# Optimization experiments

Hardware: AMD Instinct MI355X
Metric: run time of the kernel (lower is better)

Reference implementation:

```python
import jax, jax.numpy as jnp
import numpy as np
import math

N_NODES = 1048576   # total rows of x
N_SEG = 8192        # number of hyperedges (segments)
D_IN = 128
D_H = 64            # hidden_dim == embed_dim of the MHA


def setup_inputs() -> dict:
    key = jax.random.key(0)
    ks = jax.random.split(key, 12)
    x = jax.random.normal(ks[0], (N_NODES, D_IN), dtype=jnp.float32)
    # offset: sorted, with fixed endpoints 0 and N_NODES (torch.split semantics)
    cuts = jnp.sort(jax.random.randint(ks[1], (N_SEG - 1,), 0, N_NODES, dtype=jnp.int32))
    offset = jnp.concatenate([jnp.zeros((1,), jnp.int32), cuts,
                              jnp.full((1,), N_NODES, jnp.int32)])
    s1 = 1.0 / math.sqrt(D_IN)
    s2 = 1.0 / math.sqrt(D_H)
    W1 = jax.random.normal(ks[2], (D_H, D_IN), jnp.float32) * s1
    b1 = jax.random.normal(ks[3], (D_H,), jnp.float32) * s1
    W2 = jax.random.normal(ks[4], (D_H, D_H), jnp.float32) * s2
    b2 = jax.random.normal(ks[5], (D_H,), jnp.float32) * s2
    in_proj_w = jax.random.normal(ks[6], (3 * D_H, D_H), jnp.float32) * s2
    in_proj_b = jax.random.normal(ks[7], (3 * D_H,), jnp.float32) * s2
    out_w = jax.random.normal(ks[8], (D_H, D_H), jnp.float32) * s2
    out_b = jax.random.normal(ks[9], (D_H,), jnp.float32) * s2
    return {"x": x, "offset": offset, "W1": W1, "b1": b1, "W2": W2, "b2": b2,
            "in_proj_w": in_proj_w, "in_proj_b": in_proj_b,
            "out_w": out_w, "out_b": out_b}


def reference(x, offset, W1, b1, W2, b2, in_proj_w, in_proj_b, out_w, out_b):
    n = x.shape[0]
    n_seg = offset.shape[0] - 1
    # phi MLP: Linear->ReLU->Linear->ReLU
    h = jax.nn.relu(x @ W1.T + b1)
    h = jax.nn.relu(h @ W2.T + b2)                      # [N, 64]
    # ragged segment-sum pooling (torch.split + per-slice sum, fused)
    seg_ids = jnp.searchsorted(offset, jnp.arange(n, dtype=offset.dtype),
                               side='right') - 1
    tokens = jax.ops.segment_sum(h, seg_ids, num_segments=n_seg)  # [S, 64]
    # MultiheadAttention with batch_first=False: input is [L=1, batch=S, E=64],
    # so each token attends over a length-1 sequence.
    Wq, Wk, Wv = jnp.split(in_proj_w, 3, axis=0)
    bq, bk, bv = jnp.split(in_proj_b, 3, axis=0)
    t = tokens[:, None, :]                               # [S, 1, E]
    q = t @ Wq.T + bq
    k = t @ Wk.T + bk
    v = t @ Wv.T + bv
    scale = 1.0 / math.sqrt(t.shape[-1])
    scores = jnp.einsum('sqe,ske->sqk', q, k) * scale    # [S, 1, 1]
    attn = jax.nn.softmax(scores, axis=-1)               # trivially ones
    ctx = jnp.einsum('sqk,ske->sqe', attn, v)[:, 0]      # [S, 64]
    return ctx @ out_w.T + out_b
```

## Files before the change

kernel.cpp:

```cpp
#include <hip/hip_runtime.h>
#include <math.h>

#define NNODES 1048576
#define NSEG   8192
#define DIN    128
#define DH     64

typedef __bf16 bf16x8 __attribute__((ext_vector_type(8)));
typedef float  f32x4  __attribute__((ext_vector_type(4)));

__global__ void seg_fill_kernel(const int* __restrict__ offset, int* __restrict__ seg_id) {
    int s = blockIdx.x;
    int start = offset[s], end = offset[s + 1];
    for (int i = start + (int)threadIdx.x; i < end; i += (int)blockDim.x) seg_id[i] = s;
}

__global__ void fold_kernel(const float* __restrict__ in_proj_w, const float* __restrict__ in_proj_b,
                            const float* __restrict__ out_w, const float* __restrict__ out_b,
                            float* __restrict__ Mt, float* __restrict__ bfold) {
    int t = blockIdx.x * blockDim.x + threadIdx.x;
    int i = t >> 6, j = t & 63;
    const float* Wv = in_proj_w + 2 * DH * DH;
    float sum = 0.f;
#pragma unroll 8
    for (int k = 0; k < DH; ++k) sum += out_w[i * DH + k] * Wv[k * DH + j];
    Mt[j * DH + i] = sum;
    if (t < DH) {
        const float* bv = in_proj_b + 2 * DH;
        float s2 = out_b[t];
#pragma unroll 8
        for (int k = 0; k < DH; ++k) s2 += out_w[t * DH + k] * bv[k];
        bfold[t] = s2;
    }
}

__launch_bounds__(256, 2)
__global__ void mlp_seg_kernel(const float* __restrict__ x, const int* __restrict__ seg_id,
                               const float* __restrict__ W1, const float* __restrict__ b1,
                               const float* __restrict__ W2, const float* __restrict__ b2,
                               float* __restrict__ tokens) {
    const int tid  = threadIdx.x;
    const int w    = tid >> 6;
    const int lane = tid & 63;
    const int quad = lane >> 4;
    const int col  = lane & 15;

    __shared__ __align__(16) __bf16 h1buf[4][16][80];

    bf16x8 w1f[4][4];
#pragma unroll
    for (int nt = 0; nt < 4; ++nt)
#pragma unroll
        for (int kt = 0; kt < 4; ++kt) {
            const float* wp = W1 + (nt * 16 + col) * DIN + kt * 32 + quad * 8;
#pragma unroll
            for (int j = 0; j < 8; ++j) w1f[nt][kt][j] = (__bf16)wp[j];
        }
    bf16x8 w2f[4][2];
#pragma unroll
    for (int nt = 0; nt < 4; ++nt)
#pragma unroll
        for (int kt = 0; kt < 2; ++kt) {
            const float* wp = W2 + (nt * 16 + col) * DH + kt * 32 + quad * 8;
#pragma unroll
            for (int j = 0; j < 8; ++j) w2f[nt][kt][j] = (__bf16)wp[j];
        }
    float b1v[4], b2v[4];
#pragma unroll
    for (int nt = 0; nt < 4; ++nt) {
        b1v[nt] = b1[nt * 16 + col];
        b2v[nt] = b2[nt * 16 + col];
    }

#pragma unroll
    for (int sub = 0; sub < 4; ++sub) {
        const int node_base = blockIdx.x * 256 + w * 64 + sub * 16;

        const float4* xp = (const float4*)(x + (size_t)(node_base + col) * DIN + quad * 8);
        bf16x8 a[4];
#pragma unroll
        for (int kt = 0; kt < 4; ++kt) {
            float4 u  = xp[kt * 8];
            float4 v2 = xp[kt * 8 + 1];
            a[kt][0] = (__bf16)u.x;  a[kt][1] = (__bf16)u.y;
            a[kt][2] = (__bf16)u.z;  a[kt][3] = (__bf16)u.w;
            a[kt][4] = (__bf16)v2.x; a[kt][5] = (__bf16)v2.y;
            a[kt][6] = (__bf16)v2.z; a[kt][7] = (__bf16)v2.w;
        }
        int seg_lane = seg_id[node_base + col];

        f32x4 acc1[4];
#pragma unroll
        for (int nt = 0; nt < 4; ++nt) acc1[nt] = (f32x4){0.f, 0.f, 0.f, 0.f};
#pragma unroll
        for (int kt = 0; kt < 4; ++kt)
#pragma unroll
            for (int nt = 0; nt < 4; ++nt)
                acc1[nt] = __builtin_amdgcn_mfma_f32_16x16x32_bf16(a[kt], w1f[nt][kt], acc1[nt], 0, 0, 0);

#pragma unroll
        for (int nt = 0; nt < 4; ++nt)
#pragma unroll
            for (int r = 0; r < 4; ++r) {
                float v = fmaxf(acc1[nt][r] + b1v[nt], 0.f);
                h1buf[w][quad * 4 + r][nt * 16 + col] = (__bf16)v;
            }

        bf16x8 a2[2];
#pragma unroll
        for (int kt = 0; kt < 2; ++kt)
            a2[kt] = *(const bf16x8*)&h1buf[w][col][kt * 32 + quad * 8];

        f32x4 acc2[4];
#pragma unroll
        for (int nt = 0; nt < 4; ++nt) acc2[nt] = (f32x4){0.f, 0.f, 0.f, 0.f};
#pragma unroll
        for (int kt = 0; kt < 2; ++kt)
#pragma unroll
            for (int nt = 0; nt < 4; ++nt)
                acc2[nt] = __builtin_amdgcn_mfma_f32_16x16x32_bf16(a2[kt], w2f[nt][kt], acc2[nt], 0, 0, 0);

        float hv[4][4];
#pragma unroll
        for (int nt = 0; nt < 4; ++nt)
#pragma unroll
            for (int r = 0; r < 4; ++r)
                hv[nt][r] = fmaxf(acc2[nt][r] + b2v[nt], 0.f);

        int s0 = __shfl(seg_lane, 0);
        int s1 = __shfl(seg_lane, 15);
        if (s0 == s1) {
            float p[4];
#pragma unroll
            for (int nt = 0; nt < 4; ++nt) {
                p[nt] = hv[nt][0] + hv[nt][1] + hv[nt][2] + hv[nt][3];
                p[nt] += __shfl_xor(p[nt], 16);
                p[nt] += __shfl_xor(p[nt], 32);
            }
            float val = (quad == 0) ? p[0] : (quad == 1) ? p[1] : (quad == 2) ? p[2] : p[3];
            atomicAdd(&tokens[s0 * DH + quad * 16 + col], val);
        } else {
            int segs[4];
#pragma unroll
            for (int r = 0; r < 4; ++r) segs[r] = __shfl(seg_lane, quad * 4 + r);
#pragma unroll
            for (int nt = 0; nt < 4; ++nt)
#pragma unroll
                for (int r = 0; r < 4; ++r)
                    atomicAdd(&tokens[segs[r] * DH + nt * 16 + col], hv[nt][r]);
        }
    }
}

__global__ void out_kernel(const float* __restrict__ tokens, const float* __restrict__ Mt,
                           const float* __restrict__ bfold, float* __restrict__ out) {
    __shared__ float mt[DH * DH];
    __shared__ float bf[DH];
    for (int i = threadIdx.x; i < DH * DH; i += 256) mt[i] = Mt[i];
    if (threadIdx.x < DH) bf[threadIdx.x] = bfold[threadIdx.x];
    __syncthreads();
    int sl = threadIdx.x >> 6;
    int d  = threadIdx.x & 63;
    int s  = blockIdx.x * 4 + sl;
    const float* trow = tokens + s * DH;
    float sum = bf[d];
#pragma unroll 16
    for (int k = 0; k < DH; ++k) sum += trow[k] * mt[k * DH + d];
    out[s * DH + d] = sum;
}

extern "C" void kernel_launch(void* const* d_in, const int* in_sizes, int n_in,
                              void* d_out, int out_size, void* d_ws, size_t ws_size,
                              hipStream_t stream) {
    const float* x         = (const float*)d_in[0];
    const int*   offset    = (const int*)d_in[1];
    const float* W1        = (const float*)d_in[2];
    const float* b1        = (const float*)d_in[3];
    const float* W2        = (const float*)d_in[4];
    const float* b2        = (const float*)d_in[5];
    const float* in_proj_w = (const float*)d_in[6];
    const float* in_proj_b = (const float*)d_in[7];
    const float* out_w     = (const float*)d_in[8];
    const float* out_b     = (const float*)d_in[9];
    float* out = (float*)d_out;

    char* ws = (char*)d_ws;
    float* tokens = (float*)ws;
    int*   seg_id = (int*)(ws + (size_t)NSEG * DH * 4);
    float* Mt     = (float*)(ws + (size_t)NSEG * DH * 4 + (size_t)NNODES * 4);
    float* bfold  = Mt + DH * DH;

    hipMemsetAsync(tokens, 0, (size_t)NSEG * DH * sizeof(float), stream);
    seg_fill_kernel<<<NSEG, 64, 0, stream>>>(offset, seg_id);
    fold_kernel<<<16, 256, 0, stream>>>(in_proj_w, in_proj_b, out_w, out_b, Mt, bfold);
    mlp_seg_kernel<<<NNODES / 256, 256, 0, stream>>>(x, seg_id, W1, b1, W2, b2, tokens);
    out_kernel<<<NSEG / 4, 256, 0, stream>>>(tokens, Mt, bfold, out);
}
```

Before: 818.4 us.

## Double-buffer x tiles into LDS via async global_load_lds and transpose MFMA

Loads each wave's x rows through asynchronous global-to-LDS copies into two buffers, with explicit vmcnt waits, so the next 16-row tile arrives while the current one is being computed. Swaps the MFMA operands so the layer-1 output lands with four contiguous features per lane, allowing vectorized bf16x4 stores to a smaller LDS buffer. Also loads segment ids once per wave and folds the tokens memset into seg_fill_kernel to save a launch. The cost is 64 KB of LDS per block, which may limit occupancy, plus reliance on hand-written waitcnt ordering.

```diff
diff --git a/kernel.cpp b/kernel.cpp
--- a/kernel.cpp
+++ b/kernel.cpp
@@ -7,10 +7,13 @@
 #define DH     64
 
 typedef __bf16 bf16x8 __attribute__((ext_vector_type(8)));
+typedef __bf16 bf16x4 __attribute__((ext_vector_type(4)));
 typedef float  f32x4  __attribute__((ext_vector_type(4)));
 
-__global__ void seg_fill_kernel(const int* __restrict__ offset, int* __restrict__ seg_id) {
+__global__ void seg_fill_kernel(const int* __restrict__ offset, int* __restrict__ seg_id,
+                                float* __restrict__ tokens) {
     int s = blockIdx.x;
+    tokens[s * DH + (int)threadIdx.x] = 0.f;
     int start = offset[s], end = offset[s + 1];
     for (int i = start + (int)threadIdx.x; i < end; i += (int)blockDim.x) seg_id[i] = s;
 }
@@ -34,6 +37,15 @@
     }
 }
 
+__device__ __forceinline__ void stage16x8(const char* src_lane, float* lds_base) {
+#pragma unroll
+    for (int i = 0; i < 8; ++i)
+        __builtin_amdgcn_global_load_lds(
+            (const __attribute__((address_space(1))) void*)(src_lane + i * 64),
+            (__attribute__((address_space(3))) void*)((char*)lds_base + i * 1024),
+            16, 0, 0);
+}
+
 __launch_bounds__(256, 2)
 __global__ void mlp_seg_kernel(const float* __restrict__ x, const int* __restrict__ seg_id,
                                const float* __restrict__ W1, const float* __restrict__ b1,
@@ -45,7 +57,8 @@
     const int quad = lane >> 4;
     const int col  = lane & 15;
 
-    __shared__ __align__(16) __bf16 h1buf[4][16][80];
+    __shared__ __align__(16) float  xstage[4][2][2048];
+    __shared__ __align__(16) __bf16 h1w[4][16][72];
 
     bf16x8 w1f[4][4];
 #pragma unroll
@@ -65,29 +78,42 @@
 #pragma unroll
             for (int j = 0; j < 8; ++j) w2f[nt][kt][j] = (__bf16)wp[j];
         }
-    float b1v[4], b2v[4];
+    float4 b1q[4];
+    float  b2v[4];
 #pragma unroll
     for (int nt = 0; nt < 4; ++nt) {
-        b1v[nt] = b1[nt * 16 + col];
+        b1q[nt] = *(const float4*)(b1 + nt * 16 + quad * 4);
         b2v[nt] = b2[nt * 16 + col];
     }
 
-#pragma unroll
-    for (int sub = 0; sub < 4; ++sub) {
-        const int node_base = blockIdx.x * 256 + w * 64 + sub * 16;
-
-        const float4* xp = (const float4*)(x + (size_t)(node_base + col) * DIN + quad * 8);
+    const int nb0 = blockIdx.x * 256 + w * 64;
+    const int seg_all = seg_id[nb0 + lane];
+
+    const char* src0 = (const char*)(x + (size_t)(nb0 + col) * DIN + quad * 4);
+
+    float* sbuf0 = &xstage[w][0][0];
+    float* sbuf1 = &xstage[w][1][0];
+    stage16x8(src0,        sbuf0);
+    stage16x8(src0 + 8192, sbuf1);
+
+#pragma unroll
+    for (int t = 0; t < 4; ++t) {
+        if (t < 3) asm volatile("s_waitcnt vmcnt(8)" ::: "memory");
+        else       asm volatile("s_waitcnt vmcnt(0)" ::: "memory");
+        __builtin_amdgcn_sched_barrier(0);
+
+        const float4* sb = (const float4*)((t & 1) ? sbuf1 : sbuf0);
+
         bf16x8 a[4];
 #pragma unroll
         for (int kt = 0; kt < 4; ++kt) {
-            float4 u  = xp[kt * 8];
-            float4 v2 = xp[kt * 8 + 1];
+            float4 u  = sb[(kt * 8 + quad * 2) * 16 + col];
+            float4 v2 = sb[(kt * 8 + quad * 2 + 1) * 16 + col];
             a[kt][0] = (__bf16)u.x;  a[kt][1] = (__bf16)u.y;
             a[kt][2] = (__bf16)u.z;  a[kt][3] = (__bf16)u.w;
             a[kt][4] = (__bf16)v2.x; a[kt][5] = (__bf16)v2.y;
             a[kt][6] = (__bf16)v2.z; a[kt][7] = (__bf16)v2.w;
         }
-        int seg_lane = seg_id[node_base + col];
 
         f32x4 acc1[4];
 #pragma unroll
@@ -96,20 +122,21 @@
         for (int kt = 0; kt < 4; ++kt)
 #pragma unroll
             for (int nt = 0; nt < 4; ++nt)
-                acc1[nt] = __builtin_amdgcn_mfma_f32_16x16x32_bf16(a[kt], w1f[nt][kt], acc1[nt], 0, 0, 0);
-
-#pragma unroll
-        for (int nt = 0; nt < 4; ++nt)
-#pragma unroll
-            for (int r = 0; r < 4; ++r) {
-                float v = fmaxf(acc1[nt][r] + b1v[nt], 0.f);
-                h1buf[w][quad * 4 + r][nt * 16 + col] = (__bf16)v;
-            }
+                acc1[nt] = __builtin_amdgcn_mfma_f32_16x16x32_bf16(w1f[nt][kt], a[kt], acc1[nt], 0, 0, 0);
+
+#pragma unroll
+        for (int nt = 0; nt < 4; ++nt) {
+            bf16x4 hw;
+#pragma unroll
+            for (int r = 0; r < 4; ++r)
+                hw[r] = (__bf16)fmaxf(acc1[nt][r] + ((const float*)&b1q[nt])[r], 0.f);
+            *(bf16x4*)&h1w[w][col][nt * 16 + quad * 4] = hw;
+        }
 
         bf16x8 a2[2];
 #pragma unroll
         for (int kt = 0; kt < 2; ++kt)
-            a2[kt] = *(const bf16x8*)&h1buf[w][col][kt * 32 + quad * 8];
+            a2[kt] = *(const bf16x8*)&h1w[w][col][kt * 32 + quad * 8];
 
         f32x4 acc2[4];
 #pragma unroll
@@ -127,8 +154,8 @@
             for (int r = 0; r < 4; ++r)
                 hv[nt][r] = fmaxf(acc2[nt][r] + b2v[nt], 0.f);
 
-        int s0 = __shfl(seg_lane, 0);
-        int s1 = __shfl(seg_lane, 15);
+        int s0 = __shfl(seg_all, t * 16);
+        int s1 = __shfl(seg_all, t * 16 + 15);
         if (s0 == s1) {
             float p[4];
 #pragma unroll
@@ -142,13 +169,18 @@
         } else {
             int segs[4];
 #pragma unroll
-            for (int r = 0; r < 4; ++r) segs[r] = __shfl(seg_lane, quad * 4 + r);
+            for (int r = 0; r < 4; ++r) segs[r] = __shfl(seg_all, t * 16 + quad * 4 + r);
 #pragma unroll
             for (int nt = 0; nt < 4; ++nt)
 #pragma unroll
                 for (int r = 0; r < 4; ++r)
                     atomicAdd(&tokens[segs[r] * DH + nt * 16 + col], hv[nt][r]);
         }
+
+        __builtin_amdgcn_sched_barrier(0);
+        if (t == 0) stage16x8(src0 + 2 * 8192, sbuf0);
+        if (t == 1) stage16x8(src0 + 3 * 8192, sbuf1);
+        __builtin_amdgcn_sched_barrier(0);
     }
 }
 
@@ -190,8 +222,7 @@
     float* Mt     = (float*)(ws + (size_t)NSEG * DH * 4 + (size_t)NNODES * 4);
     float* bfold  = Mt + DH * DH;
 
-    hipMemsetAsync(tokens, 0, (size_t)NSEG * DH * sizeof(float), stream);
-    seg_fill_kernel<<<NSEG, 64, 0, stream>>>(offset, seg_id);
+    seg_fill_kernel<<<NSEG, 64, 0, stream>>>(offset, seg_id, tokens);
     fold_kernel<<<16, 256, 0, stream>>>(in_proj_w, in_proj_b, out_w, out_b, Mt, bfold);
     mlp_seg_kernel<<<NNODES / 256, 256, 0, stream>>>(x, seg_id, W1, b1, W2, b2, tokens);
     out_kernel<<<NSEG / 4, 256, 0, stream>>>(tokens, Mt, bfold, out);
```

New measurement: 775.4 us. 5.2% less time.
